# Optimization experiments

Measured on AMD Instinct MI355X. Metric: run time of the kernel, lower is better.

## Reference

```python
import jax, jax.numpy as jnp
import numpy as np

B, S, D, H, DK, DFF, L = 4, 1024, 1024, 16, 64, 4096, 128

def setup_inputs() -> dict:
    key = jax.random.key(0)
    ks = jax.random.split(key, 20)
    stdv = 1.0 / np.sqrt(D)
    u = lambda k, shape, s=stdv: jax.random.uniform(k, shape, jnp.float32, -s, s)
    x = jax.random.normal(ks[0], (B, S, D), jnp.float32)
    causal = jnp.triu(jnp.ones((S, S), bool), 1)          # True = masked
    attn_mask = jnp.broadcast_to(causal, (B, S, S))
    return {
        "x": x,
        "attn_mask": attn_mask,
        "W_q": u(ks[1], (H * DK, D)), "b_q": jnp.zeros((H * DK,)),
        "W_k": u(ks[2], (H * DK, D)), "b_k": jnp.zeros((H * DK,)),
        "W_v": u(ks[3], (H * DK, D)), "b_v": jnp.zeros((H * DK,)),
        "W_o": u(ks[4], (D, H * DK)), "b_o": jnp.zeros((D,)),
        "W_rel": u(ks[5], (2 * L + 1, DK), 1.0 / np.sqrt(DK)),
        "ln1_alpha": jnp.ones((D,)), "ln1_bias": jnp.zeros((D,)),
        "ln2_alpha": jnp.ones((D,)), "ln2_bias": jnp.zeros((D,)),
        "W1": u(ks[6], (DFF, D)), "b1": jnp.zeros((DFF,)),
        "W2": u(ks[7], (D, DFF)), "b2": jnp.zeros((D,)),
    }

def _layer_norm(x, alpha, bias, eps=1e-5):
    # Faithful to source: (x - mean) / (std + eps), std is biased (unbiased=False)
    m = jnp.mean(x, axis=-1, keepdims=True)
    std = jnp.sqrt(jnp.mean((x - m) ** 2, axis=-1, keepdims=True))
    return alpha * (x - m) / (std + eps) + bias

def reference(x, attn_mask, W_q, b_q, W_k, b_k, W_v, b_v, W_o, b_o, W_rel,
              ln1_alpha, ln1_bias, ln2_alpha, ln2_bias, W1, b1, W2, b2):
    b, s, d = x.shape
    q = (x @ W_q.T + b_q).reshape(b, s, H, DK)
    k = (x @ W_k.T + b_k).reshape(b, s, H, DK)
    v = (x @ W_v.T + b_v).reshape(b, s, H, DK)
    # relative position bias table lookup -> [s, s, DK]
    idx = jnp.clip(jnp.arange(s)[:, None] - jnp.arange(s)[None, :], -L, L) + L
    pos = W_rel[idx]
    # NOTE: original uses rel_pos_k_emb for BOTH pos_key and pos_value (as in source).
    scores = jnp.einsum('bqnd,bknd->bnqk', q, k) + jnp.einsum('bqnd,qkd->bnqk', q, pos)
    scores = scores / np.sqrt(DK)
    scores = jnp.where(attn_mask[:, None, :, :], jnp.float32(-10000.0), scores)
    attn = jax.nn.softmax(scores, axis=-1)
    out = jnp.einsum('bnqk,bknd->bnqd', attn, v) + jnp.einsum('bnqk,qkd->bnqd', attn, pos)
    out = out.transpose(0, 2, 1, 3).reshape(b, s, H * DK)
    out = out @ W_o.T + b_o
    # post-LN transformer layer: LN(x + attn), then LN(h + FFN(h))
    h = _layer_norm(x + out, ln1_alpha, ln1_bias)
    f = jax.nn.relu(h @ W1.T + b1) @ W2.T + b2
    return _layer_norm(h + f, ln2_alpha, ln2_bias)
```

## Files before the change

kernel.cpp:

```cpp
#include <hip/hip_runtime.h>
#include <cmath>
#include <cstdint>

typedef __bf16 bf16;
typedef __bf16 bf16x8 __attribute__((ext_vector_type(8)));
typedef __bf16 bf16x4 __attribute__((ext_vector_type(4)));
typedef float f32x4 __attribute__((ext_vector_type(4)));

__device__ __forceinline__ void async_ld16(const void* g, void* l) {
  __builtin_amdgcn_global_load_lds(
      (__attribute__((address_space(1))) void*)(uintptr_t)g,
      (__attribute__((address_space(3))) void*)l, 16, 0, 0);
}

__global__ __launch_bounds__(256) void cast_all(
    const float* __restrict__ x,  const float* __restrict__ wq, const float* __restrict__ wk,
    const float* __restrict__ wv, const float* __restrict__ wo, const float* __restrict__ w1,
    const float* __restrict__ w2,
    bf16* xb, bf16* wqb, bf16* wkb, bf16* wvb, bf16* wob, bf16* w1b, bf16* w2b)
{
  int i = blockIdx.x * 256 + threadIdx.x;
  const int M1 = 1 << 20, Q = 1 << 18;
  const float* src; bf16* dst; int off;
  if      (i < M1)            { src = x;  dst = xb;  off = i; }
  else if (i < M1 + Q)        { src = wq; dst = wqb; off = i - M1; }
  else if (i < M1 + 2 * Q)    { src = wk; dst = wkb; off = i - M1 - Q; }
  else if (i < M1 + 3 * Q)    { src = wv; dst = wvb; off = i - M1 - 2 * Q; }
  else if (i < M1 + 4 * Q)    { src = wo; dst = wob; off = i - M1 - 3 * Q; }
  else if (i < 3 * M1)        { src = w1; dst = w1b; off = i - M1 - 4 * Q; }
  else                        { src = w2; dst = w2b; off = i - 3 * M1; }
  float4 v = ((const float4*)src)[off];
  bf16x4 o; o[0]=(bf16)v.x; o[1]=(bf16)v.y; o[2]=(bf16)v.z; o[3]=(bf16)v.w;
  ((bf16x4*)dst)[off] = o;
}

template<int BM>
__device__ __forceinline__ void gemm_core(
    const bf16* __restrict__ A, const bf16* __restrict__ Bm, const float* __restrict__ bias,
    float* __restrict__ outF, bf16* __restrict__ outB,
    const float* __restrict__ residF, const bf16* __restrict__ residB,
    int N, int kld, int kbeg, int kend, int relu, bf16* As, bf16* Bs)
{
  constexpr int MI = BM / 32;
  const int tid  = threadIdx.x;
  const int wave = tid >> 6, lane = tid & 63;
  const int lr = lane & 15, lq = lane >> 4;
  const int bm = blockIdx.x * BM, bn = blockIdx.y * 128;
  const int wm = (wave >> 1) * (BM / 2), wn = (wave & 1) * 64;
  const int srow = lane >> 2, scol = (lane & 3) * 8;

  const f32x4 fz = {0.f, 0.f, 0.f, 0.f};
  f32x4 acc[MI][4];
#pragma unroll
  for (int i = 0; i < MI; i++)
#pragma unroll
    for (int j = 0; j < 4; j++) acc[i][j] = fz;

  for (int k0 = kbeg; k0 < kend; k0 += 32) {
    __syncthreads();
    if (BM == 128) {
#pragma unroll
      for (int cc = 0; cc < 2; ++cc) {
        int c = wave * 2 + cc;
        async_ld16(A + (size_t)(bm + c * 16 + srow) * kld + k0 + scol, As + c * 512);
      }
    } else {
      async_ld16(A + (size_t)(bm + wave * 16 + srow) * kld + k0 + scol, As + wave * 512);
    }
#pragma unroll
    for (int cc = 0; cc < 2; ++cc) {
      int c = wave * 2 + cc;
      async_ld16(Bm + (size_t)(bn + c * 16 + srow) * kld + k0 + scol, Bs + c * 512);
    }
    __syncthreads();
    bf16x8 af[MI], bfr[4];
#pragma unroll
    for (int mi = 0; mi < MI; mi++) af[mi]  = *(const bf16x8*)(As + (wm + mi*16 + lr)*32 + lq*8);
#pragma unroll
    for (int ni = 0; ni < 4; ni++) bfr[ni] = *(const bf16x8*)(Bs + (wn + ni*16 + lr)*32 + lq*8);
#pragma unroll
    for (int mi = 0; mi < MI; mi++)
#pragma unroll
      for (int ni = 0; ni < 4; ni++)
        acc[mi][ni] = __builtin_amdgcn_mfma_f32_16x16x32_bf16(af[mi], bfr[ni], acc[mi][ni], 0, 0, 0);
  }

#pragma unroll
  for (int ni = 0; ni < 4; ni++) {
    int n = bn + wn + ni*16 + lr;
    float bv = bias ? bias[n] : 0.0f;
#pragma unroll
    for (int mi = 0; mi < MI; mi++) {
#pragma unroll
      for (int r = 0; r < 4; r++) {
        int m = bm + wm + mi*16 + lq*4 + r;
        size_t idx = (size_t)m * N + n;
        float v = acc[mi][ni][r] + bv;
        if (relu) v = fmaxf(v, 0.0f);
        if (residF) v += residF[idx];
        if (residB) v += (float)residB[idx];
        if (outF) outF[idx] = v;
        else      outB[idx] = (bf16)v;
      }
    }
  }
}

template<int BM>
__global__ __launch_bounds__(256) void gemm_bt(
    const bf16* A, const bf16* Bm, const float* bias,
    float* outF, bf16* outB, const float* residF, const bf16* residB,
    int N, int K, int relu)
{
  __shared__ bf16 As[BM * 32];
  __shared__ bf16 Bs[128 * 32];
  gemm_core<BM>(A, Bm, bias, outF, outB, residF, residB, N, K, 0, K, relu, As, Bs);
}

__global__ __launch_bounds__(256) void gemm_splitk(
    const bf16* A, const bf16* Bm, float* part, int N, int kld, int kchunk)
{
  __shared__ bf16 As[128 * 32];
  __shared__ bf16 Bs[128 * 32];
  const int z = blockIdx.z;
  gemm_core<128>(A, Bm, nullptr, part + (size_t)z * 4096 * N, nullptr, nullptr, nullptr,
                 N, kld, z * kchunk, (z + 1) * kchunk, 0, As, Bs);
}

__global__ __launch_bounds__(256) void gemm_qkv(
    const bf16* A, const bf16* Bq, const bf16* Bk, const bf16* Bv,
    const float* bq, const float* bk, const float* bv,
    bf16* Oq, bf16* Ok, bf16* Ov, int N, int K)
{
  __shared__ bf16 As[128 * 32];
  __shared__ bf16 Bs[128 * 32];
  const bf16* Bm  = blockIdx.z == 0 ? Bq : (blockIdx.z == 1 ? Bk : Bv);
  const float* bi = blockIdx.z == 0 ? bq : (blockIdx.z == 1 ? bk : bv);
  bf16* O         = blockIdx.z == 0 ? Oq : (blockIdx.z == 1 ? Ok : Ov);
  gemm_core<128>(A, Bm, bi, nullptr, O, nullptr, nullptr, N, K, 0, K, 0, As, Bs);
}

#define S_LEN 1024
#define ROWSTR 1024

__global__ __launch_bounds__(256) void attn_kernel(
    const bf16* __restrict__ Qg, const bf16* __restrict__ Kg, const bf16* __restrict__ Vg,
    const float* __restrict__ Wrel, bf16* __restrict__ Og)
{
  __shared__ __align__(16) bf16 hist[64][136];
  __shared__ __align__(16) bf16 rel_s[64][132];
  __shared__ __align__(16) bf16 ovl[13824];
  bf16* K_s = ovl;
  bf16* V_T = ovl + 4608;
  bf16* p_s = ovl + 9216;
  bf16* Wr_n = ovl;
  bf16* Wr_t = ovl;

  const int tid = threadIdx.x;
  const int wave = tid >> 6, lane = tid & 63;
  const int lr = lane & 15, lq = lane >> 4;
  const int qblk = 15 - blockIdx.x;
  const int b = blockIdx.y >> 4, h = blockIdx.y & 15;
  const int q0 = qblk * 64;
  const int T = qblk + 1;
  const int nearStart = (T > 3) ? T - 3 : 0;
  const size_t rowbase = (size_t)b * S_LEN * ROWSTR + h * 64;

  for (int e = tid; e < 144 * 64; e += 256) {
    int t = e >> 6, d = e & 63;
    float v = (t <= 128) ? Wrel[(size_t)(128 + t) * 64 + d] : 0.0f;
    Wr_n[t * 72 + d] = (bf16)v;
  }
  for (int e = tid; e < 64 * 68; e += 256) ((uint*)hist)[e] = 0u;

  const int qfrow = q0 + wave * 16 + lr;
  bf16x8 qf[2];
#pragma unroll
  for (int c = 0; c < 2; c++)
    qf[c] = *(const bf16x8*)(Qg + rowbase + (size_t)qfrow * ROWSTR + c * 32 + lq * 8);

  __syncthreads();

  const f32x4 fz = {0.f, 0.f, 0.f, 0.f};
#pragma unroll
  for (int tt = 0; tt < 9; ++tt) {
    f32x4 a = fz;
#pragma unroll
    for (int c = 0; c < 2; c++) {
      bf16x8 wf = *(const bf16x8*)(Wr_n + (tt * 16 + lr) * 72 + c * 32 + lq * 8);
      a = __builtin_amdgcn_mfma_f32_16x16x32_bf16(qf[c], wf, a, 0, 0, 0);
    }
    int t = tt * 16 + lr;
    if (t < 132) {
#pragma unroll
      for (int r = 0; r < 4; r++) rel_s[wave * 16 + lq * 4 + r][t] = (bf16)a[r];
    }
  }
  asm volatile("s_waitcnt lgkmcnt(0)" ::: "memory");
  float relc[4];
#pragma unroll
  for (int r = 0; r < 4; r++) relc[r] = 0.125f * (float)rel_s[wave * 16 + lq * 4 + r][128];

  float l_i[4], h128[4];
  f32x4 acc_o[4];
#pragma unroll
  for (int r = 0; r < 4; r++) { l_i[r] = 0.0f; h128[r] = 0.0f; }
#pragma unroll
  for (int dt = 0; dt < 4; dt++) acc_o[dt] = fz;
  const int qrow0 = q0 + wave * 16 + lq * 4;

  const int kr0 = tid >> 3, kc0 = (tid & 7) * 8;
  const int vr0 = 2 * (tid & 31), vd0 = (tid >> 5) * 8;
  uint4 ka, kb, va, vb;
  {
    const bf16* kp = Kg + rowbase + (size_t)kr0 * ROWSTR + kc0;
    ka = *(const uint4*)kp; kb = *(const uint4*)(kp + 32 * ROWSTR);
    const bf16* vp = Vg + rowbase + (size_t)vr0 * ROWSTR + vd0;
    va = *(const uint4*)vp; vb = *(const uint4*)(vp + ROWSTR);
  }

  for (int kt = 0; kt < T; ++kt) {
    const int k0 = kt * 64;
    __syncthreads();
    *(uint4*)(K_s + kr0 * 72 + kc0) = ka;
    *(uint4*)(K_s + (kr0 + 32) * 72 + kc0) = kb;
    {
      const ushort* pa = (const ushort*)&va;
      const ushort* pb = (const ushort*)&vb;
#pragma unroll
      for (int j = 0; j < 8; j++) {
        uint w = (uint)pa[j] | ((uint)pb[j] << 16);
        *(uint*)(V_T + (vd0 + j) * 72 + vr0) = w;
      }
    }
    __syncthreads();
    if (kt + 1 < T) {
      const bf16* kp = Kg + rowbase + (size_t)(k0 + 64 + kr0) * ROWSTR + kc0;
      ka = *(const uint4*)kp; kb = *(const uint4*)(kp + 32 * ROWSTR);
      const bf16* vp = Vg + rowbase + (size_t)(k0 + 64 + vr0) * ROWSTR + vd0;
      va = *(const uint4*)vp; vb = *(const uint4*)(vp + ROWSTR);
    }

    f32x4 sc[4];
#pragma unroll
    for (int nt = 0; nt < 4; nt++) {
      sc[nt] = fz;
#pragma unroll
      for (int c = 0; c < 2; c++) {
        bf16x8 kf = *(const bf16x8*)(K_s + (nt * 16 + lr) * 72 + c * 32 + lq * 8);
        sc[nt] = __builtin_amdgcn_mfma_f32_16x16x32_bf16(qf[c], kf, sc[nt], 0, 0, 0);
      }
    }

    float pw[4][4];
    if (kt < nearStart) {
#pragma unroll
      for (int nt = 0; nt < 4; nt++)
#pragma unroll
        for (int r = 0; r < 4; r++)
          pw[nt][r] = __expf(fmaf(sc[nt][r], 0.125f, relc[r]));
#pragma unroll
      for (int r = 0; r < 4; r++) {
        float s4 = pw[0][r] + pw[1][r] + pw[2][r] + pw[3][r];
        l_i[r] += s4; h128[r] += s4;
      }
    } else {
#pragma unroll
      for (int nt = 0; nt < 4; nt++) {
        int kg = k0 + nt * 16 + lr;
#pragma unroll
        for (int r = 0; r < 4; r++) {
          int qg = qrow0 + r;
          float p = 0.0f;
          if (kg <= qg) {
            int t = qg - kg; int tc = t > 128 ? 128 : t;
            p = __expf((sc[nt][r] + (float)rel_s[wave * 16 + lq * 4 + r][tc]) * 0.125f);
            l_i[r] += p;
            if (t >= 128) h128[r] += p;
            else          hist[wave * 16 + lq * 4 + r][t] = (bf16)p;
          }
          pw[nt][r] = p;
        }
      }
    }

#pragma unroll
    for (int nt = 0; nt < 4; nt++)
#pragma unroll
      for (int r = 0; r < 4; r++)
        p_s[(wave * 16 + lq * 4 + r) * 72 + nt * 16 + lr] = (bf16)pw[nt][r];
    asm volatile("s_waitcnt lgkmcnt(0)" ::: "memory");
#pragma unroll
    for (int c = 0; c < 2; c++) {
      bf16x8 pf = *(const bf16x8*)(p_s + (wave * 16 + lr) * 72 + c * 32 + lq * 8);
#pragma unroll
      for (int dt = 0; dt < 4; dt++) {
        bf16x8 vf = *(const bf16x8*)(V_T + (dt * 16 + lr) * 72 + c * 32 + lq * 8);
        acc_o[dt] = __builtin_amdgcn_mfma_f32_16x16x32_bf16(pf, vf, acc_o[dt], 0, 0, 0);
      }
    }
  }

  __syncthreads();
  for (int e = tid; e < 64 * 128; e += 256) {
    int d = e >> 7, t = e & 127;
    Wr_t[d * 136 + t] = (bf16)Wrel[(size_t)(128 + t) * 64 + d];
  }
  __syncthreads();
#pragma unroll
  for (int c = 0; c < 4; c++) {
    bf16x8 hf = *(const bf16x8*)&hist[wave * 16 + lr][c * 32 + lq * 8];
#pragma unroll
    for (int dt = 0; dt < 4; dt++) {
      bf16x8 wf = *(const bf16x8*)(Wr_t + (dt * 16 + lr) * 136 + c * 32 + lq * 8);
      acc_o[dt] = __builtin_amdgcn_mfma_f32_16x16x32_bf16(hf, wf, acc_o[dt], 0, 0, 0);
    }
  }
#pragma unroll
  for (int mk = 1; mk <= 8; mk <<= 1)
#pragma unroll
    for (int r = 0; r < 4; r++) {
      h128[r] += __shfl_xor(h128[r], mk);
      l_i[r]  += __shfl_xor(l_i[r],  mk);
    }
#pragma unroll
  for (int dt = 0; dt < 4; dt++) {
    float wv = Wrel[(size_t)256 * 64 + dt * 16 + lr];
#pragma unroll
    for (int r = 0; r < 4; r++) acc_o[dt][r] += h128[r] * wv;
  }
#pragma unroll
  for (int dt = 0; dt < 4; dt++)
#pragma unroll
    for (int r = 0; r < 4; r++) {
      int qg = qrow0 + r;
      float v = acc_o[dt][r] / l_i[r];
      Og[rowbase + (size_t)qg * ROWSTR + dt * 16 + lr] = (bf16)v;
    }
}

__global__ __launch_bounds__(256) void ln_fuse(
    const float* __restrict__ pA, const float* __restrict__ pB,
    const float* __restrict__ bias,
    const float* __restrict__ residF, const bf16* __restrict__ residB,
    const float* __restrict__ alpha, const float* __restrict__ beta,
    float* __restrict__ outF, bf16* __restrict__ outB)
{
  const int row = blockIdx.x, tid = threadIdx.x;
  const int lane = tid & 63, wave = tid >> 6;
  const size_t base = (size_t)row * 1024;
  float4 v = ((const float4*)(pA + base))[tid];
  float4 v2 = ((const float4*)(pB + base))[tid];
  v.x += v2.x; v.y += v2.y; v.z += v2.z; v.w += v2.w;
  float4 bv = ((const float4*)bias)[tid];
  v.x += bv.x; v.y += bv.y; v.z += bv.z; v.w += bv.w;
  if (residF) {
    float4 rv = ((const float4*)(residF + base))[tid];
    v.x += rv.x; v.y += rv.y; v.z += rv.z; v.w += rv.w;
  }
  if (residB) {
    bf16x4 rv = ((const bf16x4*)(residB + base))[tid];
    v.x += (float)rv[0]; v.y += (float)rv[1]; v.z += (float)rv[2]; v.w += (float)rv[3];
  }
  float s  = v.x + v.y + v.z + v.w;
  float ss = v.x*v.x + v.y*v.y + v.z*v.z + v.w*v.w;
#pragma unroll
  for (int off = 32; off; off >>= 1) { s += __shfl_down(s, off); ss += __shfl_down(ss, off); }
  __shared__ float rs[4], rss[4];
  if (lane == 0) { rs[wave] = s; rss[wave] = ss; }
  __syncthreads();
  s  = rs[0] + rs[1] + rs[2] + rs[3];
  ss = rss[0] + rss[1] + rss[2] + rss[3];
  float mean = s * (1.0f / 1024.0f);
  float var  = ss * (1.0f / 1024.0f) - mean * mean;
  float inv  = 1.0f / (sqrtf(fmaxf(var, 0.0f)) + 1e-5f);
  float4 a = ((const float4*)alpha)[tid];
  float4 bb = ((const float4*)beta)[tid];
  float o0 = a.x * (v.x - mean) * inv + bb.x;
  float o1 = a.y * (v.y - mean) * inv + bb.y;
  float o2 = a.z * (v.z - mean) * inv + bb.z;
  float o3 = a.w * (v.w - mean) * inv + bb.w;
  if (outF) { float4 o = {o0, o1, o2, o3}; ((float4*)(outF + base))[tid] = o; }
  if (outB) { bf16x4 o; o[0]=(bf16)o0; o[1]=(bf16)o1; o[2]=(bf16)o2; o[3]=(bf16)o3;
              ((bf16x4*)(outB + base))[tid] = o; }
}

extern "C" void kernel_launch(void* const* d_in, const int* in_sizes, int n_in,
                              void* d_out, int out_size, void* d_ws, size_t ws_size,
                              hipStream_t stream) {
  (void)in_sizes; (void)n_in; (void)out_size; (void)ws_size;
  const int D = 1024, DFF = 4096;

  const float* x    = (const float*)d_in[0];
  const float* Wq   = (const float*)d_in[2];
  const float* bq   = (const float*)d_in[3];
  const float* Wk   = (const float*)d_in[4];
  const float* bk   = (const float*)d_in[5];
  const float* Wv   = (const float*)d_in[6];
  const float* bv   = (const float*)d_in[7];
  const float* Wo   = (const float*)d_in[8];
  const float* bo   = (const float*)d_in[9];
  const float* Wrel = (const float*)d_in[10];
  const float* g1   = (const float*)d_in[11];
  const float* be1  = (const float*)d_in[12];
  const float* g2   = (const float*)d_in[13];
  const float* be2  = (const float*)d_in[14];
  const float* W1   = (const float*)d_in[15];
  const float* b1   = (const float*)d_in[16];
  const float* W2   = (const float*)d_in[17];
  const float* b2   = (const float*)d_in[18];

  char* ws = (char*)d_ws;
  const size_t MB = 1024 * 1024;
  bf16*  xb   = (bf16*)(ws + 0);
  bf16*  Wqb  = (bf16*)(ws + 8  * MB);
  bf16*  Wkb  = (bf16*)(ws + 10 * MB);
  bf16*  Wvb  = (bf16*)(ws + 12 * MB);
  bf16*  Wob  = (bf16*)(ws + 14 * MB);
  bf16*  W1b  = (bf16*)(ws + 16 * MB);
  bf16*  W2b  = (bf16*)(ws + 24 * MB);
  bf16*  Qb   = (bf16*)(ws + 32 * MB);
  bf16*  Kb   = (bf16*)(ws + 40 * MB);
  bf16*  Vb   = (bf16*)(ws + 48 * MB);
  bf16*  AOb  = (bf16*)(ws + 56 * MB);
  float* part = (float*)(ws + 64 * MB);
  bf16*  f1   = Qb;
  bf16*  hb   = xb;

  cast_all<<<16384, 256, 0, stream>>>(x, Wq, Wk, Wv, Wo, W1, W2,
                                      xb, Wqb, Wkb, Wvb, Wob, W1b, W2b);

  gemm_qkv<<<dim3(32, 8, 3), 256, 0, stream>>>(xb, Wqb, Wkb, Wvb, bq, bk, bv, Qb, Kb, Vb, D, D);
  attn_kernel<<<dim3(16, 64), 256, 0, stream>>>(Qb, Kb, Vb, Wrel, AOb);
  gemm_splitk<<<dim3(32, 8, 2), 256, 0, stream>>>(AOb, Wob, part, D, D, 512);
  ln_fuse<<<4096, 256, 0, stream>>>(part, part + 4096 * 1024, bo, x, nullptr, g1, be1, nullptr, hb);
  gemm_bt<128><<<dim3(32, 32), 256, 0, stream>>>(hb, W1b, b1, nullptr, f1, nullptr, nullptr, DFF, D, 1);
  gemm_splitk<<<dim3(32, 8, 2), 256, 0, stream>>>(f1, W2b, part, D, DFF, 2048);
  ln_fuse<<<4096, 256, 0, stream>>>(part, part + 4096 * 1024, b2, nullptr, hb, g2, be2, (float*)d_out, nullptr);
}
```

Before: 417.5 us.

## Split attention tiles by key rows per wave, keep K in registers

Restructures the attention kernel so each wave owns 16 key rows and computes scores for all 64 query rows. K fragments are loaded straight from global memory into registers and prefetched one tile ahead, which removes the K shared-memory staging. QK^T is now computed before the barrier, overlapping it with the V prefetch. Row sums are combined across waves through shared memory at the end, and launch bounds request 3 blocks per CU. The cost is more registers for Q fragments, and the key-tile loop still needs two barriers.

```diff
diff --git a/kernel.cpp b/kernel.cpp
--- a/kernel.cpp
+++ b/kernel.cpp
@@ -143,18 +143,19 @@
 #define S_LEN 1024
 #define ROWSTR 1024
 
-__global__ __launch_bounds__(256) void attn_kernel(
+__global__ __launch_bounds__(256, 3) void attn_kernel(
     const bf16* __restrict__ Qg, const bf16* __restrict__ Kg, const bf16* __restrict__ Vg,
     const float* __restrict__ Wrel, bf16* __restrict__ Og)
 {
   __shared__ __align__(16) bf16 hist[64][136];
   __shared__ __align__(16) bf16 rel_s[64][132];
-  __shared__ __align__(16) bf16 ovl[13824];
-  bf16* K_s = ovl;
-  bf16* V_T = ovl + 4608;
-  bf16* p_s = ovl + 9216;
-  bf16* Wr_n = ovl;
-  bf16* Wr_t = ovl;
+  __shared__ __align__(16) bf16 vtp[9216];
+  bf16* V_T  = vtp;
+  bf16* Pb   = vtp + 4608;
+  bf16* Wst  = vtp;
+  bf16* Wr_t = vtp;
+  float* lbuf = (float*)rel_s;
+  float* hbuf = lbuf + 256;
 
   const int tid = threadIdx.x;
   const int wave = tid >> 6, lane = tid & 63;
@@ -165,143 +166,162 @@
   const int T = qblk + 1;
   const int nearStart = (T > 3) ? T - 3 : 0;
   const size_t rowbase = (size_t)b * S_LEN * ROWSTR + h * 64;
-
-  for (int e = tid; e < 144 * 64; e += 256) {
+  const f32x4 fz = {0.f, 0.f, 0.f, 0.f};
+
+  for (int e = tid; e < 128 * 64; e += 256) {
     int t = e >> 6, d = e & 63;
-    float v = (t <= 128) ? Wrel[(size_t)(128 + t) * 64 + d] : 0.0f;
-    Wr_n[t * 72 + d] = (bf16)v;
+    Wst[t * 72 + d] = (bf16)Wrel[(size_t)(128 + t) * 64 + d];
   }
   for (int e = tid; e < 64 * 68; e += 256) ((uint*)hist)[e] = 0u;
 
-  const int qfrow = q0 + wave * 16 + lr;
-  bf16x8 qf[2];
+  bf16x8 qf[4][2];
+#pragma unroll
+  for (int qt = 0; qt < 4; qt++)
+#pragma unroll
+    for (int c = 0; c < 2; c++)
+      qf[qt][c] = *(const bf16x8*)(Qg + rowbase + (size_t)(q0 + qt*16 + lr) * ROWSTR + c*32 + lq*8);
+
+  bf16x8 wb[2];
 #pragma unroll
   for (int c = 0; c < 2; c++)
-    qf[c] = *(const bf16x8*)(Qg + rowbase + (size_t)qfrow * ROWSTR + c * 32 + lq * 8);
+#pragma unroll
+    for (int j = 0; j < 8; j++)
+      wb[c][j] = (bf16)Wrel[(size_t)256 * 64 + c*32 + lq*8 + j];
 
   __syncthreads();
 
-  const f32x4 fz = {0.f, 0.f, 0.f, 0.f};
-#pragma unroll
-  for (int tt = 0; tt < 9; ++tt) {
+#pragma unroll
+  for (int tt = 0; tt < 2; ++tt)
+#pragma unroll
+    for (int qt = 0; qt < 4; ++qt) {
+      f32x4 a = fz;
+#pragma unroll
+      for (int c = 0; c < 2; c++) {
+        bf16x8 wf = *(const bf16x8*)(Wst + (wave*32 + tt*16 + lr) * 72 + c*32 + lq*8);
+        a = __builtin_amdgcn_mfma_f32_16x16x32_bf16(wf, qf[qt][c], a, 0, 0, 0);
+      }
+      bf16x4 pk; pk[0]=(bf16)a[0]; pk[1]=(bf16)a[1]; pk[2]=(bf16)a[2]; pk[3]=(bf16)a[3];
+      *(bf16x4*)(&rel_s[qt*16 + lr][wave*32 + tt*16 + lq*4]) = pk;
+    }
+  {
     f32x4 a = fz;
 #pragma unroll
-    for (int c = 0; c < 2; c++) {
-      bf16x8 wf = *(const bf16x8*)(Wr_n + (tt * 16 + lr) * 72 + c * 32 + lq * 8);
-      a = __builtin_amdgcn_mfma_f32_16x16x32_bf16(qf[c], wf, a, 0, 0, 0);
-    }
-    int t = tt * 16 + lr;
-    if (t < 132) {
-#pragma unroll
-      for (int r = 0; r < 4; r++) rel_s[wave * 16 + lq * 4 + r][t] = (bf16)a[r];
-    }
-  }
-  asm volatile("s_waitcnt lgkmcnt(0)" ::: "memory");
+    for (int c = 0; c < 2; c++)
+      a = __builtin_amdgcn_mfma_f32_16x16x32_bf16(wb[c], qf[wave][c], a, 0, 0, 0);
+    if (lq == 0) rel_s[wave*16 + lr][128] = (bf16)a[0];
+  }
+  __syncthreads();
+
   float relc[4];
 #pragma unroll
-  for (int r = 0; r < 4; r++) relc[r] = 0.125f * (float)rel_s[wave * 16 + lq * 4 + r][128];
-
-  float l_i[4], h128[4];
+  for (int qt = 0; qt < 4; qt++) relc[qt] = 0.125f * (float)rel_s[qt*16 + lr][128];
+
+  float l_p[4] = {0.f,0.f,0.f,0.f}, h_p[4] = {0.f,0.f,0.f,0.f};
   f32x4 acc_o[4];
 #pragma unroll
-  for (int r = 0; r < 4; r++) { l_i[r] = 0.0f; h128[r] = 0.0f; }
-#pragma unroll
   for (int dt = 0; dt < 4; dt++) acc_o[dt] = fz;
-  const int qrow0 = q0 + wave * 16 + lq * 4;
-
-  const int kr0 = tid >> 3, kc0 = (tid & 7) * 8;
-  const int vr0 = 2 * (tid & 31), vd0 = (tid >> 5) * 8;
-  uint4 ka, kb, va, vb;
+
+  const int vrow = 2 * (tid >> 3);
+  const int vcol = (tid & 7) * 8;
+  const int krow = 16 * wave + lr;
+
+  uint4 va, vb, va2, vb2;
+  bf16x8 kf0, kf1, kn0, kn1;
   {
-    const bf16* kp = Kg + rowbase + (size_t)kr0 * ROWSTR + kc0;
-    ka = *(const uint4*)kp; kb = *(const uint4*)(kp + 32 * ROWSTR);
-    const bf16* vp = Vg + rowbase + (size_t)vr0 * ROWSTR + vd0;
+    const bf16* vp = Vg + rowbase + (size_t)vrow * ROWSTR + vcol;
     va = *(const uint4*)vp; vb = *(const uint4*)(vp + ROWSTR);
+    const bf16* kp = Kg + rowbase + (size_t)krow * ROWSTR + lq*8;
+    kf0 = *(const bf16x8*)kp; kf1 = *(const bf16x8*)(kp + 32);
   }
 
   for (int kt = 0; kt < T; ++kt) {
     const int k0 = kt * 64;
+
+    f32x4 sc[4];
+#pragma unroll
+    for (int qt = 0; qt < 4; qt++) {
+      sc[qt] = __builtin_amdgcn_mfma_f32_16x16x32_bf16(kf0, qf[qt][0], fz, 0, 0, 0);
+      sc[qt] = __builtin_amdgcn_mfma_f32_16x16x32_bf16(kf1, qf[qt][1], sc[qt], 0, 0, 0);
+    }
+    if (kt + 1 < T) {
+      const bf16* vp = Vg + rowbase + (size_t)(k0 + 64 + vrow) * ROWSTR + vcol;
+      va2 = *(const uint4*)vp; vb2 = *(const uint4*)(vp + ROWSTR);
+      const bf16* kp = Kg + rowbase + (size_t)(k0 + 64 + krow) * ROWSTR + lq*8;
+      kn0 = *(const bf16x8*)kp; kn1 = *(const bf16x8*)(kp + 32);
+    }
+
+    float pw[4][4];
+    if (kt < nearStart) {
+#pragma unroll
+      for (int qt = 0; qt < 4; qt++) {
+#pragma unroll
+        for (int r = 0; r < 4; r++) pw[qt][r] = __expf(fmaf(sc[qt][r], 0.125f, relc[qt]));
+        float s4 = pw[qt][0] + pw[qt][1] + pw[qt][2] + pw[qt][3];
+        l_p[qt] += s4; h_p[qt] += s4;
+      }
+    } else {
+#pragma unroll
+      for (int qt = 0; qt < 4; qt++) {
+        int qg = q0 + qt*16 + lr;
+#pragma unroll
+        for (int r = 0; r < 4; r++) {
+          int kg = k0 + 16*wave + lq*4 + r;
+          float p = 0.0f;
+          if (kg <= qg) {
+            int t = qg - kg; int tc = t > 128 ? 128 : t;
+            p = __expf((sc[qt][r] + (float)rel_s[qt*16 + lr][tc]) * 0.125f);
+            l_p[qt] += p;
+            if (t >= 128) h_p[qt] += p;
+            else          hist[qt*16 + lr][t] = (bf16)p;
+          }
+          pw[qt][r] = p;
+        }
+      }
+    }
+
     __syncthreads();
-    *(uint4*)(K_s + kr0 * 72 + kc0) = ka;
-    *(uint4*)(K_s + (kr0 + 32) * 72 + kc0) = kb;
     {
       const ushort* pa = (const ushort*)&va;
       const ushort* pb = (const ushort*)&vb;
 #pragma unroll
       for (int j = 0; j < 8; j++) {
         uint w = (uint)pa[j] | ((uint)pb[j] << 16);
-        *(uint*)(V_T + (vd0 + j) * 72 + vr0) = w;
-      }
+        *(uint*)(V_T + (vcol + j) * 72 + vrow) = w;
+      }
+    }
+#pragma unroll
+    for (int qt = 0; qt < 4; qt++) {
+      bf16x4 pk; pk[0]=(bf16)pw[qt][0]; pk[1]=(bf16)pw[qt][1];
+                 pk[2]=(bf16)pw[qt][2]; pk[3]=(bf16)pw[qt][3];
+      *(bf16x4*)(Pb + (qt*16 + lr) * 72 + 16*wave + lq*4) = pk;
     }
     __syncthreads();
-    if (kt + 1 < T) {
-      const bf16* kp = Kg + rowbase + (size_t)(k0 + 64 + kr0) * ROWSTR + kc0;
-      ka = *(const uint4*)kp; kb = *(const uint4*)(kp + 32 * ROWSTR);
-      const bf16* vp = Vg + rowbase + (size_t)(k0 + 64 + vr0) * ROWSTR + vd0;
-      va = *(const uint4*)vp; vb = *(const uint4*)(vp + ROWSTR);
-    }
-
-    f32x4 sc[4];
-#pragma unroll
-    for (int nt = 0; nt < 4; nt++) {
-      sc[nt] = fz;
-#pragma unroll
-      for (int c = 0; c < 2; c++) {
-        bf16x8 kf = *(const bf16x8*)(K_s + (nt * 16 + lr) * 72 + c * 32 + lq * 8);
-        sc[nt] = __builtin_amdgcn_mfma_f32_16x16x32_bf16(qf[c], kf, sc[nt], 0, 0, 0);
-      }
-    }
-
-    float pw[4][4];
-    if (kt < nearStart) {
-#pragma unroll
-      for (int nt = 0; nt < 4; nt++)
-#pragma unroll
-        for (int r = 0; r < 4; r++)
-          pw[nt][r] = __expf(fmaf(sc[nt][r], 0.125f, relc[r]));
-#pragma unroll
-      for (int r = 0; r < 4; r++) {
-        float s4 = pw[0][r] + pw[1][r] + pw[2][r] + pw[3][r];
-        l_i[r] += s4; h128[r] += s4;
-      }
-    } else {
-#pragma unroll
-      for (int nt = 0; nt < 4; nt++) {
-        int kg = k0 + nt * 16 + lr;
-#pragma unroll
-        for (int r = 0; r < 4; r++) {
-          int qg = qrow0 + r;
-          float p = 0.0f;
-          if (kg <= qg) {
-            int t = qg - kg; int tc = t > 128 ? 128 : t;
-            p = __expf((sc[nt][r] + (float)rel_s[wave * 16 + lq * 4 + r][tc]) * 0.125f);
-            l_i[r] += p;
-            if (t >= 128) h128[r] += p;
-            else          hist[wave * 16 + lq * 4 + r][t] = (bf16)p;
-          }
-          pw[nt][r] = p;
-        }
-      }
-    }
-
-#pragma unroll
-    for (int nt = 0; nt < 4; nt++)
-#pragma unroll
-      for (int r = 0; r < 4; r++)
-        p_s[(wave * 16 + lq * 4 + r) * 72 + nt * 16 + lr] = (bf16)pw[nt][r];
-    asm volatile("s_waitcnt lgkmcnt(0)" ::: "memory");
+
 #pragma unroll
     for (int c = 0; c < 2; c++) {
-      bf16x8 pf = *(const bf16x8*)(p_s + (wave * 16 + lr) * 72 + c * 32 + lq * 8);
+      bf16x8 pf = *(const bf16x8*)(Pb + (16*wave + lr) * 72 + c*32 + lq*8);
 #pragma unroll
       for (int dt = 0; dt < 4; dt++) {
-        bf16x8 vf = *(const bf16x8*)(V_T + (dt * 16 + lr) * 72 + c * 32 + lq * 8);
+        bf16x8 vf = *(const bf16x8*)(V_T + (dt*16 + lr) * 72 + c*32 + lq*8);
         acc_o[dt] = __builtin_amdgcn_mfma_f32_16x16x32_bf16(pf, vf, acc_o[dt], 0, 0, 0);
       }
     }
-  }
-
+    kf0 = kn0; kf1 = kn1; va = va2; vb = vb2;
+  }
+
+#pragma unroll
+  for (int qt = 0; qt < 4; qt++) {
+    l_p[qt] += __shfl_xor(l_p[qt], 16); l_p[qt] += __shfl_xor(l_p[qt], 32);
+    h_p[qt] += __shfl_xor(h_p[qt], 16); h_p[qt] += __shfl_xor(h_p[qt], 32);
+  }
   __syncthreads();
+  if (lq == 0) {
+#pragma unroll
+    for (int qt = 0; qt < 4; qt++) {
+      lbuf[wave*64 + qt*16 + lr] = l_p[qt];
+      hbuf[wave*64 + qt*16 + lr] = h_p[qt];
+    }
+  }
   for (int e = tid; e < 64 * 128; e += 256) {
     int d = e >> 7, t = e & 127;
     Wr_t[d * 136 + t] = (bf16)Wrel[(size_t)(128 + t) * 64 + d];
@@ -309,33 +329,32 @@
   __syncthreads();
 #pragma unroll
   for (int c = 0; c < 4; c++) {
-    bf16x8 hf = *(const bf16x8*)&hist[wave * 16 + lr][c * 32 + lq * 8];
+    bf16x8 hf = *(const bf16x8*)&hist[wave*16 + lr][c*32 + lq*8];
 #pragma unroll
     for (int dt = 0; dt < 4; dt++) {
-      bf16x8 wf = *(const bf16x8*)(Wr_t + (dt * 16 + lr) * 136 + c * 32 + lq * 8);
+      bf16x8 wf = *(const bf16x8*)(Wr_t + (dt*16 + lr) * 136 + c*32 + lq*8);
       acc_o[dt] = __builtin_amdgcn_mfma_f32_16x16x32_bf16(hf, wf, acc_o[dt], 0, 0, 0);
     }
   }
-#pragma unroll
-  for (int mk = 1; mk <= 8; mk <<= 1)
+  float l4[4], h4[4];
+#pragma unroll
+  for (int r = 0; r < 4; r++) {
+    int q = wave*16 + lq*4 + r;
+    l4[r] = lbuf[q] + lbuf[64+q] + lbuf[128+q] + lbuf[192+q];
+    h4[r] = hbuf[q] + hbuf[64+q] + hbuf[128+q] + hbuf[192+q];
+  }
+#pragma unroll
+  for (int dt = 0; dt < 4; dt++) {
+    float wv = Wrel[(size_t)256 * 64 + dt*16 + lr];
+#pragma unroll
+    for (int r = 0; r < 4; r++) acc_o[dt][r] += h4[r] * wv;
+  }
+#pragma unroll
+  for (int dt = 0; dt < 4; dt++)
 #pragma unroll
     for (int r = 0; r < 4; r++) {
-      h128[r] += __shfl_xor(h128[r], mk);
-      l_i[r]  += __shfl_xor(l_i[r],  mk);
-    }
-#pragma unroll
-  for (int dt = 0; dt < 4; dt++) {
-    float wv = Wrel[(size_t)256 * 64 + dt * 16 + lr];
-#pragma unroll
-    for (int r = 0; r < 4; r++) acc_o[dt][r] += h128[r] * wv;
-  }
-#pragma unroll
-  for (int dt = 0; dt < 4; dt++)
-#pragma unroll
-    for (int r = 0; r < 4; r++) {
-      int qg = qrow0 + r;
-      float v = acc_o[dt][r] / l_i[r];
-      Og[rowbase + (size_t)qg * ROWSTR + dt * 16 + lr] = (bf16)v;
+      int qg = q0 + wave*16 + lq*4 + r;
+      Og[rowbase + (size_t)qg * ROWSTR + dt*16 + lr] = (bf16)(acc_o[dt][r] / l4[r]);
     }
 }
 
```

After: 414.8 us. No clear change (-0.7%).
